# Performance work log

Measured on AMD Instinct MI355X. Metric: run time of the kernel, lower is better.

## Reference

```python
import jax, jax.numpy as jnp
import numpy as np

D_MODEL = 1024
NUM_HEADS = 16
D_HEAD = D_MODEL // NUM_HEADS


def setup_inputs() -> dict:
    key = jax.random.key(0)
    ks = jax.random.split(key, 9)
    s = 1.0 / np.sqrt(D_MODEL)
    return {
        "x": jax.random.normal(ks[0], (4, 2048, D_MODEL), dtype=jnp.float32),
        "Wq": jax.random.normal(ks[1], (D_MODEL, D_MODEL), dtype=jnp.float32) * s,
        "bq": jnp.zeros((D_MODEL,), dtype=jnp.float32),
        "Wk": jax.random.normal(ks[2], (D_MODEL, D_MODEL), dtype=jnp.float32) * s,
        "bk": jnp.zeros((D_MODEL,), dtype=jnp.float32),
        "Wv": jax.random.normal(ks[3], (D_MODEL, D_MODEL), dtype=jnp.float32) * s,
        "bv": jnp.zeros((D_MODEL,), dtype=jnp.float32),
        "Wo": jax.random.normal(ks[4], (D_MODEL, D_MODEL), dtype=jnp.float32) * s,
        "bo": jnp.zeros((D_MODEL,), dtype=jnp.float32),
    }


def reference(x, Wq, bq, Wk, bk, Wv, bv, Wo, bo):
    B, S, _ = x.shape
    # projections (torch Linear: y = x @ W^T + b; here W stored as [in, out])
    q = (x @ Wq + bq).reshape(B, S, NUM_HEADS, D_HEAD).transpose(0, 2, 1, 3)
    k = (x @ Wk + bk).reshape(B, S, NUM_HEADS, D_HEAD).transpose(0, 2, 1, 3)
    v = (x @ Wv + bv).reshape(B, S, NUM_HEADS, D_HEAD).transpose(0, 2, 1, 3)
    scale = 1.0 / jnp.sqrt(jnp.asarray(D_HEAD, dtype=x.dtype))
    scores = jnp.einsum("bhqd,bhkd->bhqk", q, k) * scale  # [B,H,S,S]
    attn = jax.nn.softmax(scores, axis=-1)
    ctx = jnp.einsum("bhqk,bhkd->bhqd", attn, v)  # [B,H,S,Dh]
    ctx = ctx.transpose(0, 2, 1, 3).reshape(B, S, D_MODEL)
    return ctx @ Wo + bo
```

## Files before the change

kernel.cpp:

```cpp
#include <hip/hip_runtime.h>
#include <hip/hip_bf16.h>

#define DM 1024
#define NH 16
#define DH 64
#define BB 4
#define SS 2048
#define MROWS (BB*SS)

typedef unsigned short u16;
typedef short bf16x8 __attribute__((ext_vector_type(8)));
typedef float f32x4 __attribute__((ext_vector_type(4)));

#define MFMA16(a, b, c) __builtin_amdgcn_mfma_f32_16x16x32_bf16((a), (b), (c), 0, 0, 0)

__device__ __forceinline__ u16 f2bf(float f) {
  union { float f; unsigned u; } v; v.f = f;
  unsigned u = v.u;
  return (u16)((u + 0x7fffu + ((u >> 16) & 1u)) >> 16);
}

__device__ __forceinline__ bf16x8 ld_bf8(const u16* p) {
  return *(const bf16x8*)p;
}

__global__ __launch_bounds__(256) void k_cvt_x(const float* __restrict__ x,
                                               u16* __restrict__ xb) {
  int i = (blockIdx.x * 256 + threadIdx.x) * 4;
  float4 v = *(const float4*)(x + i);
  ushort4 o;
  o.x = f2bf(v.x); o.y = f2bf(v.y); o.z = f2bf(v.z); o.w = f2bf(v.w);
  *(ushort4*)(xb + i) = o;
}

__global__ __launch_bounds__(1024) void k_tw(const float* __restrict__ Wq,
                                             const float* __restrict__ Wk,
                                             const float* __restrict__ Wv,
                                             const float* __restrict__ Wo,
                                             u16* __restrict__ Wt) {
  __shared__ float t[32][33];
  int k0 = blockIdx.x * 32;
  int seg = blockIdx.y >> 5;
  int n0 = (blockIdx.y & 31) * 32;
  const float* W = seg == 0 ? Wq : seg == 1 ? Wk : seg == 2 ? Wv : Wo;
  int tx = threadIdx.x, ty = threadIdx.y;
  t[ty][tx] = W[(size_t)(k0 + ty) * DM + n0 + tx];
  __syncthreads();
  Wt[(size_t)(seg * DM + n0 + ty) * DM + k0 + tx] = f2bf(t[tx][ty]);
}

__global__ __launch_bounds__(256) void k_gemm(
    const u16* __restrict__ A, const u16* __restrict__ Bt,
    int M, int N, int K,
    const float* __restrict__ b0, const float* __restrict__ b1,
    const float* __restrict__ b2,
    u16* __restrict__ oq, u16* __restrict__ ok, u16* __restrict__ ov,
    float* __restrict__ of, int mode) {
  __shared__ __align__(16) u16 As[128][40];
  __shared__ __align__(16) u16 Bs[128][40];
  int tid = threadIdx.x;
  int wave = tid >> 6, lane = tid & 63, quad = lane >> 4, l16 = lane & 15;
  int bm = blockIdx.x * 128, bn = blockIdx.y * 128;
  int wr = (wave >> 1) * 64, wc = (wave & 1) * 64;
  f32x4 acc[4][4] = {};

  for (int k0 = 0; k0 < K; k0 += 32) {
#pragma unroll
    for (int i = 0; i < 2; ++i) {
      int c = i * 256 + tid;
      int r = c >> 2, col = (c & 3) * 8;
      *(bf16x8*)(&As[r][col]) = ld_bf8(A + (size_t)(bm + r) * K + k0 + col);
      *(bf16x8*)(&Bs[r][col]) = ld_bf8(Bt + (size_t)(bn + r) * K + k0 + col);
    }
    __syncthreads();
    bf16x8 af[4], bfr[4];
#pragma unroll
    for (int mi = 0; mi < 4; ++mi)
      af[mi] = *(const bf16x8*)(&As[wr + mi * 16 + l16][quad * 8]);
#pragma unroll
    for (int ni = 0; ni < 4; ++ni)
      bfr[ni] = *(const bf16x8*)(&Bs[wc + ni * 16 + l16][quad * 8]);
#pragma unroll
    for (int mi = 0; mi < 4; ++mi)
#pragma unroll
      for (int ni = 0; ni < 4; ++ni)
        acc[mi][ni] = MFMA16(af[mi], bfr[ni], acc[mi][ni]);
    __syncthreads();
  }

  if (mode == 0) {
#pragma unroll
    for (int mi = 0; mi < 4; ++mi)
#pragma unroll
      for (int ni = 0; ni < 4; ++ni)
#pragma unroll
        for (int r = 0; r < 4; ++r) {
          int row = bm + wr + mi * 16 + quad * 4 + r;
          int col = bn + wc + ni * 16 + l16;
          of[(size_t)row * N + col] = acc[mi][ni][r] + b0[col];
        }
  } else {
    int seg = bn >> 10;
    const float* bia = seg == 0 ? b0 : seg == 1 ? b1 : b2;
    int cb = bn & 1023;
    if (seg == 2) {
#pragma unroll
      for (int mi = 0; mi < 4; ++mi)
#pragma unroll
        for (int ni = 0; ni < 4; ++ni) {
          int row = bm + wr + mi * 16 + quad * 4;
          int col = cb + wc + ni * 16 + l16;
          float bv_ = bia[col];
          int bb2 = row >> 11, s = row & 2047, hh = col >> 6, dh = col & 63;
          ushort4 o4;
          o4.x = f2bf(acc[mi][ni][0] + bv_);
          o4.y = f2bf(acc[mi][ni][1] + bv_);
          o4.z = f2bf(acc[mi][ni][2] + bv_);
          o4.w = f2bf(acc[mi][ni][3] + bv_);
          *(ushort4*)(&ov[(((size_t)bb2 * NH + hh) * DH + dh) * SS + s]) = o4;
        }
    } else {
      u16* o = seg == 0 ? oq : ok;
      float sc = seg == 0 ? (0.125f * 1.44269504f) : 1.0f;
#pragma unroll
      for (int mi = 0; mi < 4; ++mi)
#pragma unroll
        for (int ni = 0; ni < 4; ++ni)
#pragma unroll
          for (int r = 0; r < 4; ++r) {
            int row = bm + wr + mi * 16 + quad * 4 + r;
            int col = cb + wc + ni * 16 + l16;
            float v = (acc[mi][ni][r] + bia[col]) * sc;
            int bb2 = row >> 11, s = row & 2047, hh = col >> 6, dh = col & 63;
            o[((((size_t)bb2 * NH + hh) * SS) + s) * DH + dh] = f2bf(v);
          }
    }
  }
}

__global__ __launch_bounds__(256) void k_attn(const u16* __restrict__ Q,
                                              const u16* __restrict__ Kg,
                                              const u16* __restrict__ VT,
                                              u16* __restrict__ ctx) {
  __shared__ __align__(16) u16 Ks[2][64][72];
  __shared__ __align__(16) u16 Vts[2][64][72];
  __shared__ __align__(16) u16 Ps[4][32][72];
  int tid = threadIdx.x;
  int wave = tid >> 6, lane = tid & 63, quad = lane >> 4, l16 = lane & 15;
  int q0 = blockIdx.x * 128;
  int h = blockIdx.y, b = blockIdx.z;
  size_t bh = ((size_t)b * NH + h) * SS * DH;
  const u16* Qp = Q + bh + (size_t)(q0 + wave * 32) * DH;
  const u16* Kp = Kg + bh;
  const u16* Vp = VT + ((size_t)b * NH + h) * DH * SS;

  bf16x8 qf[2][2];
#pragma unroll
  for (int m = 0; m < 2; ++m) {
    qf[m][0] = ld_bf8(Qp + (m * 16 + l16) * DH + quad * 8);
    qf[m][1] = ld_bf8(Qp + (m * 16 + l16) * DH + 32 + quad * 8);
  }

  f32x4 O[2][4] = {};
  float lrun[2][4] = {};

  int sr = tid >> 3;
  int sc = (tid & 7) * 8;

#pragma unroll
  for (int i = 0; i < 2; ++i) {
    int r = sr + i * 32;
    *(bf16x8*)(&Ks[0][r][sc]) = ld_bf8(Kp + (size_t)r * DH + sc);
    *(bf16x8*)(&Vts[0][r][sc]) = ld_bf8(Vp + (size_t)r * SS + sc);
  }
  __syncthreads();

  for (int it = 0; it < SS / 64; ++it) {
    int p = it & 1;
    int kv1 = (it + 1) * 64;

    f32x4 s[2][4];
#pragma unroll
    for (int t = 0; t < 4; ++t) {
      bf16x8 kb0 = *(const bf16x8*)(&Ks[p][t * 16 + l16][quad * 8]);
      bf16x8 kb1 = *(const bf16x8*)(&Ks[p][t * 16 + l16][32 + quad * 8]);
#pragma unroll
      for (int m = 0; m < 2; ++m) {
        f32x4 z = {};
        z = MFMA16(qf[m][0], kb0, z);
        z = MFMA16(qf[m][1], kb1, z);
        s[m][t] = z;
      }
    }

    if (kv1 < SS) {
#pragma unroll
      for (int i = 0; i < 2; ++i) {
        int r = sr + i * 32;
        *(bf16x8*)(&Ks[1 - p][r][sc]) =
            ld_bf8(Kp + (size_t)(kv1 + r) * DH + sc);
        *(bf16x8*)(&Vts[1 - p][r][sc]) =
            ld_bf8(Vp + (size_t)r * SS + kv1 + sc);
      }
    }

#pragma unroll
    for (int m = 0; m < 2; ++m)
#pragma unroll
      for (int t = 0; t < 4; ++t)
#pragma unroll
        for (int r = 0; r < 4; ++r) {
          float pv = exp2f(s[m][t][r]);
          lrun[m][r] += pv;
          Ps[wave][m * 16 + quad * 4 + r][t * 16 + l16] = f2bf(pv);
        }

    bf16x8 pf[2][2];
#pragma unroll
    for (int m = 0; m < 2; ++m) {
      pf[m][0] = *(const bf16x8*)(&Ps[wave][m * 16 + l16][quad * 8]);
      pf[m][1] = *(const bf16x8*)(&Ps[wave][m * 16 + l16][32 + quad * 8]);
    }
#pragma unroll
    for (int c = 0; c < 4; ++c) {
      bf16x8 v0 = *(const bf16x8*)(&Vts[p][c * 16 + l16][quad * 8]);
      bf16x8 v1 = *(const bf16x8*)(&Vts[p][c * 16 + l16][32 + quad * 8]);
#pragma unroll
      for (int m = 0; m < 2; ++m) {
        O[m][c] = MFMA16(pf[m][0], v0, O[m][c]);
        O[m][c] = MFMA16(pf[m][1], v1, O[m][c]);
      }
    }
    __syncthreads();
  }

  float inv[2][4];
#pragma unroll
  for (int m = 0; m < 2; ++m)
#pragma unroll
    for (int r = 0; r < 4; ++r) {
      float l = lrun[m][r];
#pragma unroll
      for (int off = 1; off < 16; off <<= 1) l += __shfl_xor(l, off);
      inv[m][r] = 1.0f / l;
    }
#pragma unroll
  for (int m = 0; m < 2; ++m) {
    size_t ob = ((size_t)b * SS + q0 + wave * 32 + m * 16) * DM + h * DH;
#pragma unroll
    for (int c = 0; c < 4; ++c)
#pragma unroll
      for (int r = 0; r < 4; ++r)
        ctx[ob + (size_t)(quad * 4 + r) * DM + c * 16 + l16] =
            f2bf(O[m][c][r] * inv[m][r]);
  }
}

extern "C" void kernel_launch(void* const* d_in, const int* in_sizes, int n_in,
                              void* d_out, int out_size, void* d_ws, size_t ws_size,
                              hipStream_t stream) {
  const float* x  = (const float*)d_in[0];
  const float* Wq = (const float*)d_in[1];
  const float* bq = (const float*)d_in[2];
  const float* Wk = (const float*)d_in[3];
  const float* bk = (const float*)d_in[4];
  const float* Wv = (const float*)d_in[5];
  const float* bv = (const float*)d_in[6];
  const float* Wo = (const float*)d_in[7];
  const float* bo = (const float*)d_in[8];
  float* out = (float*)d_out;

  char* ws = (char*)d_ws;
  u16* xb = (u16*)(ws);
  u16* Wt = (u16*)(ws + (16u << 20));
  u16* Qb = (u16*)(ws + (24u << 20));
  u16* Kb = (u16*)(ws + (40u << 20));
  u16* VT = (u16*)(ws + (56u << 20));
  u16* Cb = (u16*)(ws + (72u << 20));

  k_cvt_x<<<MROWS * DM / 1024, 256, 0, stream>>>(x, xb);
  k_tw<<<dim3(32, 128), dim3(32, 32), 0, stream>>>(Wq, Wk, Wv, Wo, Wt);
  k_gemm<<<dim3(MROWS / 128, 24), 256, 0, stream>>>(
      xb, Wt, MROWS, 3 * DM, DM, bq, bk, bv, Qb, Kb, VT, nullptr, 1);
  k_attn<<<dim3(SS / 128, NH, BB), 256, 0, stream>>>(Qb, Kb, VT, Cb);
  k_gemm<<<dim3(MROWS / 128, 8), 256, 0, stream>>>(
      Cb, Wt + (size_t)3 * DM * DM, MROWS, DM, DM, bo, nullptr, nullptr,
      nullptr, nullptr, nullptr, out, 0);
}
```

Before: 381.2 us.

## Keep softmax probabilities in registers by computing transposed S = K·Qᵀ

The attention kernel swaps the MFMA operand order so each lane holds score values whose layout matches the B operand of a 16x16x16 MFMA. The probabilities are packed to bf16 in registers and fed straight into the P·V product, which removes the per-wave LDS staging buffer and its store/reload round trip. The output accumulator becomes transposed (O^T), and row sums now need only two cross-lane shuffles. The trade is that P·V moves from the K=32 to the K=16 MFMA instruction, doubling its instruction count, and ctx stores become 8-byte packed writes.

```diff
diff --git a/kernel.cpp b/kernel.cpp
--- a/kernel.cpp
+++ b/kernel.cpp
@@ -10,14 +10,21 @@
 
 typedef unsigned short u16;
 typedef short bf16x8 __attribute__((ext_vector_type(8)));
+typedef short bf16x4 __attribute__((ext_vector_type(4)));
 typedef float f32x4 __attribute__((ext_vector_type(4)));
+typedef unsigned uintx2 __attribute__((ext_vector_type(2)));
 
 #define MFMA16(a, b, c) __builtin_amdgcn_mfma_f32_16x16x32_bf16((a), (b), (c), 0, 0, 0)
+#define MFMA16K16(a, b, c) __builtin_amdgcn_mfma_f32_16x16x16bf16_1k((a), (b), (c), 0, 0, 0)
 
 __device__ __forceinline__ u16 f2bf(float f) {
   union { float f; unsigned u; } v; v.f = f;
   unsigned u = v.u;
   return (u16)((u + 0x7fffu + ((u >> 16) & 1u)) >> 16);
+}
+
+__device__ __forceinline__ unsigned pack2bf(float a, float b) {
+  return ((unsigned)f2bf(b) << 16) | (unsigned)f2bf(a);
 }
 
 __device__ __forceinline__ bf16x8 ld_bf8(const u16* p) {
@@ -144,7 +151,6 @@
                                               u16* __restrict__ ctx) {
   __shared__ __align__(16) u16 Ks[2][64][72];
   __shared__ __align__(16) u16 Vts[2][64][72];
-  __shared__ __align__(16) u16 Ps[4][32][72];
   int tid = threadIdx.x;
   int wave = tid >> 6, lane = tid & 63, quad = lane >> 4, l16 = lane & 15;
   int q0 = blockIdx.x * 128;
@@ -156,13 +162,13 @@
 
   bf16x8 qf[2][2];
 #pragma unroll
-  for (int m = 0; m < 2; ++m) {
-    qf[m][0] = ld_bf8(Qp + (m * 16 + l16) * DH + quad * 8);
-    qf[m][1] = ld_bf8(Qp + (m * 16 + l16) * DH + 32 + quad * 8);
-  }
-
-  f32x4 O[2][4] = {};
-  float lrun[2][4] = {};
+  for (int qt = 0; qt < 2; ++qt) {
+    qf[qt][0] = ld_bf8(Qp + (qt * 16 + l16) * DH + quad * 8);
+    qf[qt][1] = ld_bf8(Qp + (qt * 16 + l16) * DH + 32 + quad * 8);
+  }
+
+  f32x4 Ot[4][2] = {};
+  float lrun[2] = {0.0f, 0.0f};
 
   int sr = tid >> 3;
   int sc = (tid & 7) * 8;
@@ -185,11 +191,11 @@
       bf16x8 kb0 = *(const bf16x8*)(&Ks[p][t * 16 + l16][quad * 8]);
       bf16x8 kb1 = *(const bf16x8*)(&Ks[p][t * 16 + l16][32 + quad * 8]);
 #pragma unroll
-      for (int m = 0; m < 2; ++m) {
+      for (int qt = 0; qt < 2; ++qt) {
         f32x4 z = {};
-        z = MFMA16(qf[m][0], kb0, z);
-        z = MFMA16(qf[m][1], kb1, z);
-        s[m][t] = z;
+        z = MFMA16(kb0, qf[qt][0], z);
+        z = MFMA16(kb1, qf[qt][1], z);
+        s[qt][t] = z;
       }
     }
 
@@ -204,55 +210,54 @@
       }
     }
 
-#pragma unroll
-    for (int m = 0; m < 2; ++m)
-#pragma unroll
-      for (int t = 0; t < 4; ++t)
-#pragma unroll
-        for (int r = 0; r < 4; ++r) {
-          float pv = exp2f(s[m][t][r]);
-          lrun[m][r] += pv;
-          Ps[wave][m * 16 + quad * 4 + r][t * 16 + l16] = f2bf(pv);
-        }
-
-    bf16x8 pf[2][2];
-#pragma unroll
-    for (int m = 0; m < 2; ++m) {
-      pf[m][0] = *(const bf16x8*)(&Ps[wave][m * 16 + l16][quad * 8]);
-      pf[m][1] = *(const bf16x8*)(&Ps[wave][m * 16 + l16][32 + quad * 8]);
-    }
-#pragma unroll
-    for (int c = 0; c < 4; ++c) {
-      bf16x8 v0 = *(const bf16x8*)(&Vts[p][c * 16 + l16][quad * 8]);
-      bf16x8 v1 = *(const bf16x8*)(&Vts[p][c * 16 + l16][32 + quad * 8]);
-#pragma unroll
-      for (int m = 0; m < 2; ++m) {
-        O[m][c] = MFMA16(pf[m][0], v0, O[m][c]);
-        O[m][c] = MFMA16(pf[m][1], v1, O[m][c]);
-      }
-    }
+    bf16x4 pb[2][4];
+#pragma unroll
+    for (int qt = 0; qt < 2; ++qt)
+#pragma unroll
+      for (int t = 0; t < 4; ++t) {
+        float e0 = exp2f(s[qt][t][0]);
+        float e1 = exp2f(s[qt][t][1]);
+        float e2 = exp2f(s[qt][t][2]);
+        float e3 = exp2f(s[qt][t][3]);
+        lrun[qt] += (e0 + e1) + (e2 + e3);
+        uintx2 w;
+        w[0] = pack2bf(e0, e1);
+        w[1] = pack2bf(e2, e3);
+        pb[qt][t] = __builtin_bit_cast(bf16x4, w);
+      }
+
+#pragma unroll
+    for (int c = 0; c < 4; ++c)
+#pragma unroll
+      for (int dt = 0; dt < 4; ++dt) {
+        bf16x4 va = *(const bf16x4*)(&Vts[p][dt * 16 + l16][c * 16 + quad * 4]);
+#pragma unroll
+        for (int qt = 0; qt < 2; ++qt)
+          Ot[dt][qt] = MFMA16K16(va, pb[qt][c], Ot[dt][qt]);
+      }
     __syncthreads();
   }
 
-  float inv[2][4];
-#pragma unroll
-  for (int m = 0; m < 2; ++m)
-#pragma unroll
-    for (int r = 0; r < 4; ++r) {
-      float l = lrun[m][r];
-#pragma unroll
-      for (int off = 1; off < 16; off <<= 1) l += __shfl_xor(l, off);
-      inv[m][r] = 1.0f / l;
-    }
-#pragma unroll
-  for (int m = 0; m < 2; ++m) {
-    size_t ob = ((size_t)b * SS + q0 + wave * 32 + m * 16) * DM + h * DH;
-#pragma unroll
-    for (int c = 0; c < 4; ++c)
-#pragma unroll
-      for (int r = 0; r < 4; ++r)
-        ctx[ob + (size_t)(quad * 4 + r) * DM + c * 16 + l16] =
-            f2bf(O[m][c][r] * inv[m][r]);
+  float inv[2];
+#pragma unroll
+  for (int qt = 0; qt < 2; ++qt) {
+    float l = lrun[qt];
+    l += __shfl_xor(l, 16);
+    l += __shfl_xor(l, 32);
+    inv[qt] = 1.0f / l;
+  }
+
+#pragma unroll
+  for (int qt = 0; qt < 2; ++qt) {
+    int q = q0 + wave * 32 + qt * 16 + l16;
+    size_t ob = ((size_t)b * SS + q) * DM + h * DH;
+#pragma unroll
+    for (int dt = 0; dt < 4; ++dt) {
+      uintx2 o;
+      o[0] = pack2bf(Ot[dt][qt][0] * inv[qt], Ot[dt][qt][1] * inv[qt]);
+      o[1] = pack2bf(Ot[dt][qt][2] * inv[qt], Ot[dt][qt][3] * inv[qt]);
+      *(uintx2*)(&ctx[ob + dt * 16 + quad * 4]) = o;
+    }
   }
 }
 
```

Result: slower. 398.4 us (+4.5%).
